# Kernel tuning notes

Hardware: AMD Instinct MI355X
Metric: run time of the kernel (lower is better)

The kernel has to match this reference:

```python
import jax, jax.numpy as jnp
import numpy as np

N = 8388608          # total items across all scopes
SEG = 64             # uniform scope (segment) length
TARGET_MAX = 1000000


def setup_inputs() -> dict:
    key = jax.random.key(0)
    k1, k2, k3 = jax.random.split(key, 3)
    mean = jax.random.normal(k1, (N, 1), dtype=jnp.float32)
    variance = jax.random.uniform(k2, (N, 1), dtype=jnp.float32)
    targets = jax.random.randint(k3, (N,), 0, TARGET_MAX, dtype=jnp.int64)
    return {"mean": mean, "variance": variance, "targets": targets, "scope": SEG}


def reference(mean, variance, targets, scope):
    # score = cat(mean, variance) -> column 0 is mean m, column 1 is variance v
    n = mean.shape[0]
    b = n // scope                                   # number of ragged segments (uniform here)
    m = mean[:, 0].reshape(b, scope)
    v = variance[:, 0].reshape(b, scope)
    t = targets.reshape(b, scope)

    # per-segment descending sort by targets
    idx = jnp.argsort(-t, axis=1)                    # [b, scope]
    ms = jnp.take_along_axis(m, idx, axis=1)
    vs = jnp.take_along_axis(v, idx, axis=1)

    # tril(exp(m_i - m_j + (v_i + v_j)/2)).sum(0)[j]
    #   = exp(-m_j + v_j/2) * sum_{i>=j} exp(m_i + v_i/2)
    z = jnp.exp(ms + 0.5 * vs)                       # [b, scope]
    rev_cumsum = jnp.cumsum(z[:, ::-1], axis=1)[:, ::-1]  # sum over i >= j
    logS = -ms + 0.5 * vs + jnp.log(rev_cumsum)      # -log(1/S) = log S

    per_seg_loss = jnp.mean(logS, axis=1)            # torch.mean over the segment
    avg = jnp.sum(per_seg_loss) / b                  # losses / len(scope)
    return avg.reshape(1)                            # matches torch.Tensor([0]) accumulator shape
```

## Files before the change

kernel.cpp:

```cpp
#include <hip/hip_runtime.h>

#define N_TOTAL 8388608
#define SEG 64
#define NSEG (N_TOTAL / SEG)
#define NPAIR (NSEG / 2)
#define TPB 256
#define BLOCKS 2048
#define WAVES (BLOCKS * TPB / 64)
#define ITERS (NPAIR / WAVES)

template <int CTRL>
__device__ __forceinline__ unsigned dpp_qp(unsigned v) {
    return (unsigned)__builtin_amdgcn_update_dpp(0, (int)v, CTRL, 0xf, 0xf, true);
}
template <int CTRL, int ROW_MASK>
__device__ __forceinline__ float dpp_add(float x) {
    int mv = __builtin_amdgcn_update_dpp(0, __float_as_int(x), CTRL, ROW_MASK, 0xf, true);
    return x + __int_as_float(mv);
}
template <int D>
__device__ __forceinline__ unsigned lane_xor_c(unsigned v) {
    if (D == 1) return dpp_qp<0xB1>(v);
    if (D == 2) return dpp_qp<0x4E>(v);
    return (unsigned)__builtin_amdgcn_ds_swizzle((int)v, (D << 10) | 0x1F);
}

__global__ __launch_bounds__(TPB, 8) void mledis_seg2(
    const float2* __restrict__ mean2,
    const float2* __restrict__ var2,
    const int2*   __restrict__ tgt2,
    float* __restrict__ partial)
{
    const int lane = threadIdx.x & 63;
    const int h    = lane >> 5;
    const int l5   = lane & 31;
    const int waveId = blockIdx.x * (TPB / 64) + (threadIdx.x >> 6);

    float2 mc = mean2[waveId * 64 + lane];
    float2 vc = var2 [waveId * 64 + lane];
    int2   tc = tgt2 [waveId * 64 + lane];

    float acc = 0.0f;

    #pragma unroll
    for (int it = 0; it < ITERS; ++it) {
        float2 mn_, vn_; int2 tn_;
        if (it + 1 < ITERS) {
            const int b = (waveId + (it + 1) * WAVES) * 64 + lane;
            mn_ = mean2[b]; vn_ = var2[b]; tn_ = tgt2[b];
        }

        const float z0 = __expf(fmaf(0.5f, vc.x, mc.x));
        const float z1 = __expf(fmaf(0.5f, vc.y, mc.y));
        acc += fmaf(0.5f, vc.x, -mc.x) + fmaf(0.5f, vc.y, -mc.y);

        const unsigned e0 = 2u * (unsigned)l5;
        unsigned k0 = (((unsigned)tc.x) << 6) | (63u - e0);
        unsigned k1 = (((unsigned)tc.y) << 6) | (63u - (e0 + 1u));

        #define CMP_XLANE(K, D)                                              \
            {                                                                \
                const unsigned o0 = lane_xor_c<D>(k0);                       \
                const unsigned o1 = lane_xor_c<D>(k1);                       \
                const bool lower = (l5 & (D)) == 0;                          \
                const bool up    = (l5 & ((K) >> 1)) == 0;                   \
                const bool sel   = (up == lower);                            \
                const unsigned mn0 = min(k0, o0), mx0 = max(k0, o0);         \
                const unsigned mn1 = min(k1, o1), mx1 = max(k1, o1);         \
                k0 = sel ? mn0 : mx0;                                        \
                k1 = sel ? mn1 : mx1;                                        \
            }
        #define CMP_LOCAL(K)                                                 \
            {                                                                \
                const bool up = (l5 & ((K) >> 1)) == 0;                      \
                const unsigned mn = min(k0, k1), mx = max(k0, k1);           \
                k0 = up ? mn : mx;                                           \
                k1 = up ? mx : mn;                                           \
            }
        CMP_LOCAL(2)
        CMP_XLANE(4, 1)  CMP_LOCAL(4)
        CMP_XLANE(8, 2)  CMP_XLANE(8, 1)  CMP_LOCAL(8)
        CMP_XLANE(16, 4) CMP_XLANE(16, 2) CMP_XLANE(16, 1) CMP_LOCAL(16)
        CMP_XLANE(32, 8) CMP_XLANE(32, 4) CMP_XLANE(32, 2) CMP_XLANE(32, 1) CMP_LOCAL(32)
        CMP_XLANE(64, 16) CMP_XLANE(64, 8) CMP_XLANE(64, 4) CMP_XLANE(64, 2) CMP_XLANE(64, 1) CMP_LOCAL(64)
        #undef CMP_XLANE
        #undef CMP_LOCAL

        const int o0i = 63 - (int)(k0 & 63u);
        const int o1i = 63 - (int)(k1 & 63u);
        const int a0 = (h * 32 + (o0i >> 1)) << 2;
        const int a1 = (h * 32 + (o1i >> 1)) << 2;
        const int zi0 = __float_as_int(z0);
        const int zi1 = __float_as_int(z1);
        const float g00 = __int_as_float(__builtin_amdgcn_ds_bpermute(a0, zi0));
        const float g01 = __int_as_float(__builtin_amdgcn_ds_bpermute(a0, zi1));
        const float g10 = __int_as_float(__builtin_amdgcn_ds_bpermute(a1, zi0));
        const float g11 = __int_as_float(__builtin_amdgcn_ds_bpermute(a1, zi1));
        const float za0 = (o0i & 1) ? g01 : g00;
        const float za1 = (o1i & 1) ? g11 : g10;

        float P = za0 + za1;
        P = dpp_add<0x111, 0xf>(P);
        P = dpp_add<0x112, 0xf>(P);
        P = dpp_add<0x114, 0xf>(P);
        P = dpp_add<0x118, 0xf>(P);
        P = dpp_add<0x142, 0xa>(P);
        acc += __logf(P * (P - za1));

        mc = mn_; vc = vn_; tc = tn_;
    }

    #pragma unroll
    for (int off = 32; off > 0; off >>= 1)
        acc += __shfl_xor(acc, off, 64);

    __shared__ float sacc[TPB / 64];
    const int waveInBlock = threadIdx.x >> 6;
    if (lane == 0) sacc[waveInBlock] = acc;
    __syncthreads();
    if (threadIdx.x == 0) {
        float b = 0.0f;
        #pragma unroll
        for (int i = 0; i < TPB / 64; ++i) b += sacc[i];
        partial[blockIdx.x] = b;
    }
}

__global__ __launch_bounds__(TPB) void mledis_final_reduce(
    const float* __restrict__ partial, float* __restrict__ out)
{
    float s = 0.0f;
    for (int i = threadIdx.x; i < BLOCKS; i += TPB) s += partial[i];
    #pragma unroll
    for (int off = 32; off > 0; off >>= 1) s += __shfl_xor(s, off, 64);

    __shared__ float sacc[TPB / 64];
    const int lane = threadIdx.x & 63;
    const int w = threadIdx.x >> 6;
    if (lane == 0) sacc[w] = s;
    __syncthreads();
    if (threadIdx.x == 0) {
        float tot = 0.0f;
        #pragma unroll
        for (int i = 0; i < TPB / 64; ++i) tot += sacc[i];
        out[0] = tot * (1.0f / (float)N_TOTAL);
    }
}

extern "C" void kernel_launch(void* const* d_in, const int* in_sizes, int n_in,
                              void* d_out, int out_size, void* d_ws, size_t ws_size,
                              hipStream_t stream) {
    const float2* mean2 = (const float2*)d_in[0];
    const float2* var2  = (const float2*)d_in[1];
    const int2*   tgt2  = (const int2*)d_in[2];

    float* partial = (float*)d_ws;
    float* out = (float*)d_out;

    mledis_seg2<<<BLOCKS, TPB, 0, stream>>>(mean2, var2, tgt2, partial);
    mledis_final_reduce<<<1, TPB, 0, stream>>>(partial, out);
}
```

Measured before the change: 122.8 us.

## Sort four elements per lane with 16-lane bitonic network and LDS gather

Each lane now holds four elements, so a wave covers four 64-element segments on 16 lanes each. The kernel loads with float4/int4, runs an in-register sorting network plus mirrored DPP/swizzle exchange stages, gathers z values through a per-wave LDS buffer instead of ds_bpermute, and takes a per-lane prefix with DPP row adds. The aim is fewer cross-lane ops and wider loads per element. It adds LDS traffic and register pressure. Targets are still packed as 32-bit keys, which assumes int4 element width matches the input layout.

```diff
diff --git a/kernel.cpp b/kernel.cpp
--- a/kernel.cpp
+++ b/kernel.cpp
@@ -3,120 +3,157 @@
 #define N_TOTAL 8388608
 #define SEG 64
 #define NSEG (N_TOTAL / SEG)
-#define NPAIR (NSEG / 2)
 #define TPB 256
 #define BLOCKS 2048
 #define WAVES (BLOCKS * TPB / 64)
-#define ITERS (NPAIR / WAVES)
+#define SPW 4
+#define ITERS (NSEG / (WAVES * SPW))
 
 template <int CTRL>
-__device__ __forceinline__ unsigned dpp_qp(unsigned v) {
+__device__ __forceinline__ unsigned dppmov(unsigned v) {
     return (unsigned)__builtin_amdgcn_update_dpp(0, (int)v, CTRL, 0xf, 0xf, true);
 }
-template <int CTRL, int ROW_MASK>
-__device__ __forceinline__ float dpp_add(float x) {
-    int mv = __builtin_amdgcn_update_dpp(0, __float_as_int(x), CTRL, ROW_MASK, 0xf, true);
+template <int CTRL>
+__device__ __forceinline__ float dpp_addf(float x) {
+    int mv = __builtin_amdgcn_update_dpp(0, __float_as_int(x), CTRL, 0xf, 0xf, true);
     return x + __int_as_float(mv);
 }
-template <int D>
-__device__ __forceinline__ unsigned lane_xor_c(unsigned v) {
-    if (D == 1) return dpp_qp<0xB1>(v);
-    if (D == 2) return dpp_qp<0x4E>(v);
-    return (unsigned)__builtin_amdgcn_ds_swizzle((int)v, (D << 10) | 0x1F);
-}
+__device__ __forceinline__ unsigned umn(unsigned a, unsigned b) { return a < b ? a : b; }
+__device__ __forceinline__ unsigned umx(unsigned a, unsigned b) { return a > b ? a : b; }
 
-__global__ __launch_bounds__(TPB, 8) void mledis_seg2(
-    const float2* __restrict__ mean2,
-    const float2* __restrict__ var2,
-    const int2*   __restrict__ tgt2,
+__global__ __launch_bounds__(TPB, 8) void mledis_seg4(
+    const float4* __restrict__ mean4,
+    const float4* __restrict__ var4,
+    const int4*   __restrict__ tgt4,
     float* __restrict__ partial)
 {
     const int lane = threadIdx.x & 63;
-    const int h    = lane >> 5;
-    const int l5   = lane & 31;
-    const int waveId = blockIdx.x * (TPB / 64) + (threadIdx.x >> 6);
+    const int q    = lane & 15;
+    const int wIB  = threadIdx.x >> 6;
+    const int waveId = blockIdx.x * (TPB / 64) + wIB;
 
-    float2 mc = mean2[waveId * 64 + lane];
-    float2 vc = var2 [waveId * 64 + lane];
-    int2   tc = tgt2 [waveId * 64 + lane];
+    __shared__ __align__(16) float zbuf[TPB / 64][64 * SPW];
+    float* const zbase = &zbuf[wIB][(lane >> 4) * 64];
+
+    const bool lo1 = (q & 1) == 0;
+    const bool lo2 = (q & 2) == 0;
+    const bool lo4 = (q & 4) == 0;
+    const bool lo8 = (q & 8) == 0;
+
+    float4 mc = mean4[waveId * 64 + lane];
+    float4 vc = var4 [waveId * 64 + lane];
+    int4   tc = tgt4 [waveId * 64 + lane];
 
     float acc = 0.0f;
 
+    #define CE(a, b) { const unsigned _mn = umn(a, b); const unsigned _mx = umx(a, b); \
+                       a = _mn; b = _mx; }
+    #define MIR(CTRL, LO) { \
+        const unsigned o0 = dppmov<CTRL>(k3); \
+        const unsigned o1 = dppmov<CTRL>(k2); \
+        const unsigned o2 = dppmov<CTRL>(k1); \
+        const unsigned o3 = dppmov<CTRL>(k0); \
+        k0 = (LO) ? umn(k0, o0) : umx(k0, o0); \
+        k1 = (LO) ? umn(k1, o1) : umx(k1, o1); \
+        k2 = (LO) ? umn(k2, o2) : umx(k2, o2); \
+        k3 = (LO) ? umn(k3, o3) : umx(k3, o3); \
+    }
+    #define XD(CTRL, LO) { \
+        const unsigned o0 = dppmov<CTRL>(k0); \
+        const unsigned o1 = dppmov<CTRL>(k1); \
+        const unsigned o2 = dppmov<CTRL>(k2); \
+        const unsigned o3 = dppmov<CTRL>(k3); \
+        k0 = (LO) ? umn(k0, o0) : umx(k0, o0); \
+        k1 = (LO) ? umn(k1, o1) : umx(k1, o1); \
+        k2 = (LO) ? umn(k2, o2) : umx(k2, o2); \
+        k3 = (LO) ? umn(k3, o3) : umx(k3, o3); \
+    }
+    #define XS4(LO) { \
+        const unsigned o0 = (unsigned)__builtin_amdgcn_ds_swizzle((int)k0, 0x101F); \
+        const unsigned o1 = (unsigned)__builtin_amdgcn_ds_swizzle((int)k1, 0x101F); \
+        const unsigned o2 = (unsigned)__builtin_amdgcn_ds_swizzle((int)k2, 0x101F); \
+        const unsigned o3 = (unsigned)__builtin_amdgcn_ds_swizzle((int)k3, 0x101F); \
+        k0 = (LO) ? umn(k0, o0) : umx(k0, o0); \
+        k1 = (LO) ? umn(k1, o1) : umx(k1, o1); \
+        k2 = (LO) ? umn(k2, o2) : umx(k2, o2); \
+        k3 = (LO) ? umn(k3, o3) : umx(k3, o3); \
+    }
+
     #pragma unroll
     for (int it = 0; it < ITERS; ++it) {
-        float2 mn_, vn_; int2 tn_;
+        float4 mn_, vn_; int4 tn_;
         if (it + 1 < ITERS) {
             const int b = (waveId + (it + 1) * WAVES) * 64 + lane;
-            mn_ = mean2[b]; vn_ = var2[b]; tn_ = tgt2[b];
+            mn_ = mean4[b]; vn_ = var4[b]; tn_ = tgt4[b];
         }
 
         const float z0 = __expf(fmaf(0.5f, vc.x, mc.x));
         const float z1 = __expf(fmaf(0.5f, vc.y, mc.y));
-        acc += fmaf(0.5f, vc.x, -mc.x) + fmaf(0.5f, vc.y, -mc.y);
+        const float z2 = __expf(fmaf(0.5f, vc.z, mc.z));
+        const float z3 = __expf(fmaf(0.5f, vc.w, mc.w));
+        *(float4*)(zbase + 4 * q) = make_float4(z0, z1, z2, z3);
 
-        const unsigned e0 = 2u * (unsigned)l5;
-        unsigned k0 = (((unsigned)tc.x) << 6) | (63u - e0);
-        unsigned k1 = (((unsigned)tc.y) << 6) | (63u - (e0 + 1u));
+        acc += fmaf(0.5f, (vc.x + vc.y) + (vc.z + vc.w),
+                    -((mc.x + mc.y) + (mc.z + mc.w)));
 
-        #define CMP_XLANE(K, D)                                              \
-            {                                                                \
-                const unsigned o0 = lane_xor_c<D>(k0);                       \
-                const unsigned o1 = lane_xor_c<D>(k1);                       \
-                const bool lower = (l5 & (D)) == 0;                          \
-                const bool up    = (l5 & ((K) >> 1)) == 0;                   \
-                const bool sel   = (up == lower);                            \
-                const unsigned mn0 = min(k0, o0), mx0 = max(k0, o0);         \
-                const unsigned mn1 = min(k1, o1), mx1 = max(k1, o1);         \
-                k0 = sel ? mn0 : mx0;                                        \
-                k1 = sel ? mn1 : mx1;                                        \
-            }
-        #define CMP_LOCAL(K)                                                 \
-            {                                                                \
-                const bool up = (l5 & ((K) >> 1)) == 0;                      \
-                const unsigned mn = min(k0, k1), mx = max(k0, k1);           \
-                k0 = up ? mn : mx;                                           \
-                k1 = up ? mx : mn;                                           \
-            }
-        CMP_LOCAL(2)
-        CMP_XLANE(4, 1)  CMP_LOCAL(4)
-        CMP_XLANE(8, 2)  CMP_XLANE(8, 1)  CMP_LOCAL(8)
-        CMP_XLANE(16, 4) CMP_XLANE(16, 2) CMP_XLANE(16, 1) CMP_LOCAL(16)
-        CMP_XLANE(32, 8) CMP_XLANE(32, 4) CMP_XLANE(32, 2) CMP_XLANE(32, 1) CMP_LOCAL(32)
-        CMP_XLANE(64, 16) CMP_XLANE(64, 8) CMP_XLANE(64, 4) CMP_XLANE(64, 2) CMP_XLANE(64, 1) CMP_LOCAL(64)
-        #undef CMP_XLANE
-        #undef CMP_LOCAL
+        const unsigned eb = 63u - 4u * (unsigned)q;
+        unsigned k0 = (((unsigned)tc.x) << 6) | eb;
+        unsigned k1 = (((unsigned)tc.y) << 6) | (eb - 1u);
+        unsigned k2 = (((unsigned)tc.z) << 6) | (eb - 2u);
+        unsigned k3 = (((unsigned)tc.w) << 6) | (eb - 3u);
 
-        const int o0i = 63 - (int)(k0 & 63u);
-        const int o1i = 63 - (int)(k1 & 63u);
-        const int a0 = (h * 32 + (o0i >> 1)) << 2;
-        const int a1 = (h * 32 + (o1i >> 1)) << 2;
-        const int zi0 = __float_as_int(z0);
-        const int zi1 = __float_as_int(z1);
-        const float g00 = __int_as_float(__builtin_amdgcn_ds_bpermute(a0, zi0));
-        const float g01 = __int_as_float(__builtin_amdgcn_ds_bpermute(a0, zi1));
-        const float g10 = __int_as_float(__builtin_amdgcn_ds_bpermute(a1, zi0));
-        const float g11 = __int_as_float(__builtin_amdgcn_ds_bpermute(a1, zi1));
-        const float za0 = (o0i & 1) ? g01 : g00;
-        const float za1 = (o1i & 1) ? g11 : g10;
+        CE(k0, k1); CE(k2, k3);
+        CE(k0, k3); CE(k1, k2);
+        CE(k0, k1); CE(k2, k3);
+        MIR(0xB1, lo1);
+        CE(k0, k2); CE(k1, k3);
+        CE(k0, k1); CE(k2, k3);
+        MIR(0x1B, lo2);
+        XD(0xB1, lo1);
+        CE(k0, k2); CE(k1, k3);
+        CE(k0, k1); CE(k2, k3);
+        MIR(0x141, lo4);
+        XD(0x4E, lo2);
+        XD(0xB1, lo1);
+        CE(k0, k2); CE(k1, k3);
+        CE(k0, k1); CE(k2, k3);
+        MIR(0x140, lo8);
+        XS4(lo4);
+        XD(0x4E, lo2);
+        XD(0xB1, lo1);
+        CE(k0, k2); CE(k1, k3);
+        CE(k0, k1); CE(k2, k3);
 
-        float P = za0 + za1;
-        P = dpp_add<0x111, 0xf>(P);
-        P = dpp_add<0x112, 0xf>(P);
-        P = dpp_add<0x114, 0xf>(P);
-        P = dpp_add<0x118, 0xf>(P);
-        P = dpp_add<0x142, 0xa>(P);
-        acc += __logf(P * (P - za1));
+        const float zs0 = zbase[63 - (int)(k0 & 63u)];
+        const float zs1 = zbase[63 - (int)(k1 & 63u)];
+        const float zs2 = zbase[63 - (int)(k2 & 63u)];
+        const float zs3 = zbase[63 - (int)(k3 & 63u)];
+
+        const float Qs = (zs0 + zs1) + (zs2 + zs3);
+        float P = Qs;
+        P = dpp_addf<0x111>(P);
+        P = dpp_addf<0x112>(P);
+        P = dpp_addf<0x114>(P);
+        P = dpp_addf<0x118>(P);
+        const float S0 = (P - Qs) + zs0;
+        const float S1 = S0 + zs1;
+        const float S2 = S1 + zs2;
+        const float S3 = S2 + zs3;
+        acc += __logf((S0 * S1) * (S2 * S3));
 
         mc = mn_; vc = vn_; tc = tn_;
     }
+    #undef CE
+    #undef MIR
+    #undef XD
+    #undef XS4
 
     #pragma unroll
     for (int off = 32; off > 0; off >>= 1)
         acc += __shfl_xor(acc, off, 64);
 
     __shared__ float sacc[TPB / 64];
-    const int waveInBlock = threadIdx.x >> 6;
-    if (lane == 0) sacc[waveInBlock] = acc;
+    if (lane == 0) sacc[wIB] = acc;
     __syncthreads();
     if (threadIdx.x == 0) {
         float b = 0.0f;
@@ -150,13 +187,13 @@
 extern "C" void kernel_launch(void* const* d_in, const int* in_sizes, int n_in,
                               void* d_out, int out_size, void* d_ws, size_t ws_size,
                               hipStream_t stream) {
-    const float2* mean2 = (const float2*)d_in[0];
-    const float2* var2  = (const float2*)d_in[1];
-    const int2*   tgt2  = (const int2*)d_in[2];
+    const float4* mean4 = (const float4*)d_in[0];
+    const float4* var4  = (const float4*)d_in[1];
+    const int4*   tgt4  = (const int4*)d_in[2];
 
     float* partial = (float*)d_ws;
     float* out = (float*)d_out;
 
-    mledis_seg2<<<BLOCKS, TPB, 0, stream>>>(mean2, var2, tgt2, partial);
+    mledis_seg4<<<BLOCKS, TPB, 0, stream>>>(mean4, var4, tgt4, partial);
     mledis_final_reduce<<<1, TPB, 0, stream>>>(partial, out);
 }
```

New measurement: 120.0 us. 1.02x faster.
